# Kernel tuning notes

Measured on AMD Instinct MI355X. Metric: run time of the kernel, lower is better.

Reference implementation:

```python
import jax, jax.numpy as jnp
import numpy as np
from jax import lax

B, N, D = 16, 2048, 256
H = 64  # hidden_dim
EPS = 1e-5


def zero_softmax(x, eps=EPS):
    # zeros stay exactly zero: exp(0)-1 == 0
    e = jnp.exp(x) - 1.0
    return e / (jnp.sum(e, axis=-1, keepdims=True) + eps)


def setup_inputs() -> dict:
    key = jax.random.key(0)
    ks = jax.random.split(key, 9)
    s_in = 1.0 / np.sqrt(D)
    x = jax.random.normal(ks[0], (B, N, D), dtype=jnp.float32)
    Wq = jax.random.uniform(ks[1], (D, H), jnp.float32, -s_in, s_in)
    bq = jax.random.uniform(ks[2], (H,), jnp.float32, -s_in, s_in)
    Wk = jax.random.uniform(ks[3], (D, H), jnp.float32, -s_in, s_in)
    bk = jax.random.uniform(ks[4], (H,), jnp.float32, -s_in, s_in)
    Wv = jax.random.uniform(ks[5], (D, H), jnp.float32, -s_in, s_in)
    bv = jax.random.uniform(ks[6], (H,), jnp.float32, -s_in, s_in)
    s_c = 1.0 / 3.0  # conv fan_in = 1*3*3 = 9
    conv_w = jax.random.uniform(ks[7], (1, 1, 3, 3), jnp.float32, -s_c, s_c)
    conv_b = jax.random.uniform(ks[8], (1,), jnp.float32, -s_c, s_c)
    return {"x": x, "Wq": Wq, "bq": bq, "Wk": Wk, "bk": bk,
            "Wv": Wv, "bv": bv, "conv_w": conv_w, "conv_b": conv_b}


def reference(x, Wq, bq, Wk, bk, Wv, bv, conv_w, conv_b):
    scale = H ** (-0.5)
    q = jnp.einsum('bnd,dh->bnh', x, Wq) + bq
    k = jnp.einsum('bnd,dh->bnh', x, Wk) + bk
    v = jnp.einsum('bnd,dh->bnh', x, Wv) + bv
    A_dense = jnp.einsum('bnh,bmh->bnm', q, k) * scale  # [B, N, N]
    A_in = A_dense[:, None, :, :]  # [B, 1, N, N]
    A_conv = lax.conv_general_dilated(
        A_in, conv_w, window_strides=(1, 1), padding='SAME',
        dimension_numbers=('NCHW', 'OIHW', 'NCHW')) + conv_b[None, :, None, None]
    A_conv = jax.nn.sigmoid(A_conv)[:, 0, :, :]
    A_sparse = jax.nn.relu(A_dense - A_conv)
    A_norm = zero_softmax(A_sparse)
    return jnp.einsum('bnm,bmh->bnh', A_norm, v)
```

## Files before the change

kernel.cpp:

```cpp
#include <hip/hip_runtime.h>
#include <hip/hip_bf16.h>

typedef __bf16 bf16_t;
typedef __bf16 bf16x8 __attribute__((ext_vector_type(8)));
typedef float  floatx4 __attribute__((ext_vector_type(4)));

#define BQ 16
#define NTOK 2048
#define DIM 256
#define HD 64

__global__ __launch_bounds__(256) void k_prep(const float* __restrict__ Wq,
                                              const float* __restrict__ Wk,
                                              const float* __restrict__ Wv,
                                              bf16_t* __restrict__ wt) {
    int o = blockIdx.x * 256 + threadIdx.x;
    int w = o >> 14;
    int r = o & 16383;
    int h = r >> 8;
    int d = r & 255;
    const float* W = (w == 0) ? Wq : ((w == 1) ? Wk : Wv);
    wt[o] = (bf16_t)W[d * 64 + h];
}

#define XS 264
__global__ __launch_bounds__(256) void k_qkv(const float* __restrict__ x,
                                             const bf16_t* __restrict__ wt,
                                             const float* __restrict__ bq,
                                             const float* __restrict__ bk,
                                             const float* __restrict__ bv,
                                             bf16_t* __restrict__ qb,
                                             bf16_t* __restrict__ kb,
                                             bf16_t* __restrict__ vt) {
    __shared__ bf16_t x_ls[64 * XS];
    __shared__ bf16_t vt_ls[64 * 72];

    int b  = blockIdx.x >> 5;
    int t0 = (blockIdx.x & 31) << 6;
    int t  = threadIdx.x;
    int lane = t & 63;
    int w    = t >> 6;
    int m_   = lane & 15;
    int q4   = lane >> 4;

    for (int tau = t; tau < 4096; tau += 256) {
        int row = tau >> 6, ch = tau & 63;
        float4 v = ((const float4*)x)[(size_t)(b * NTOK + t0 + row) * 64 + ch];
        bf16_t tmp[4] = {(bf16_t)v.x, (bf16_t)v.y, (bf16_t)v.z, (bf16_t)v.w};
        *(uint2*)(&x_ls[row * XS + ch * 4]) = *(uint2*)tmp;
    }
    __syncthreads();

    for (int wi = 0; wi < 3; ++wi) {
        const bf16_t* wtw = wt + wi * 16384;
        floatx4 acc[4];
        #pragma unroll
        for (int mt = 0; mt < 4; ++mt) acc[mt] = floatx4{0.f, 0.f, 0.f, 0.f};

        #pragma unroll
        for (int ks = 0; ks < 8; ++ks) {
            bf16x8 bfrag = *(const bf16x8*)(wtw + (16 * w + m_) * 256 + ks * 32 + q4 * 8);
            #pragma unroll
            for (int mt = 0; mt < 4; ++mt) {
                bf16x8 afrag = *(const bf16x8*)(&x_ls[(16 * mt + m_) * XS + ks * 32 + q4 * 8]);
                acc[mt] = __builtin_amdgcn_mfma_f32_16x16x32_bf16(afrag, bfrag, acc[mt], 0, 0, 0);
            }
        }
        const float* bias_p = (wi == 0) ? bq : ((wi == 1) ? bk : bv);
        float bias = bias_p[16 * w + m_];
        float scale = (wi == 0) ? 0.125f : 1.0f;

        if (wi < 2) {
            bf16_t* dst = (wi == 0) ? qb : kb;
            #pragma unroll
            for (int mt = 0; mt < 4; ++mt)
                #pragma unroll
                for (int r = 0; r < 4; ++r) {
                    int tok = t0 + 16 * mt + 4 * q4 + r;
                    dst[(size_t)(b * NTOK + tok) * 64 + 16 * w + m_] = (bf16_t)((acc[mt][r] + bias) * scale);
                }
        } else {
            #pragma unroll
            for (int mt = 0; mt < 4; ++mt)
                #pragma unroll
                for (int r = 0; r < 4; ++r)
                    vt_ls[(16 * w + m_) * 72 + 16 * mt + 4 * q4 + r] = (bf16_t)(acc[mt][r] + bias);
            __syncthreads();
            for (int tau = t; tau < 512; tau += 256) {
                int h = tau >> 3, ch = tau & 7;
                uint4 val = *(const uint4*)(&vt_ls[h * 72 + ch * 8]);
                *(uint4*)(vt + (size_t)(b * 64 + h) * NTOK + t0 + ch * 8) = val;
            }
        }
    }
}

#define SA 52
#define SP 72
#define RINT 46
#define NITER 45
__global__ __launch_bounds__(256) void k_attn(const bf16_t* __restrict__ qb,
                                              const bf16_t* __restrict__ kb,
                                              const bf16_t* __restrict__ vt,
                                              const float* __restrict__ conv_w,
                                              const float* __restrict__ conv_b,
                                              float* __restrict__ out) {
    __shared__ bf16_t q_ls[48 * SP];
    __shared__ bf16_t k_ls[48 * SP];
    __shared__ bf16_t v_ls[64 * SP];
    __shared__ float  A_ls[48 * SA];
    __shared__ bf16_t p_ls[48 * SP];
    __shared__ float  rs_ls[48];

    int b  = blockIdx.y;
    int r0 = blockIdx.x * RINT;
    int t = threadIdx.x, lane = t & 63, w = t >> 6;
    int m_ = lane & 15, q4 = lane >> 4;

    const uint* vt32 = (const uint*)vt + (size_t)b * 64 * 1024;

    int vh[6], vc[6];
    #pragma unroll
    for (int j = 0; j < 6; ++j) { int tau = t + 256 * j; vh[j] = tau / 23; vc[j] = tau % 23; }

    float cw[9];
    #pragma unroll
    for (int i = 0; i < 9; ++i) cw[i] = conv_w[i];
    float cb = conv_b[0];

    uint4 kreg[2];
    uint  vreg[6];
    auto prefetch = [&](int c0) {
        {
            int row = t >> 3, ch = t & 7;
            int g = c0 - 1 + row;
            uint4 val = make_uint4(0u, 0u, 0u, 0u);
            if (g >= 0 && g < NTOK)
                val = *(const uint4*)(kb + (size_t)(b * NTOK + g) * 64 + ch * 8);
            kreg[0] = val;
        }
        if (t < 128) {
            int row = (t + 256) >> 3, ch = t & 7;
            int g = c0 - 1 + row;
            uint4 val = make_uint4(0u, 0u, 0u, 0u);
            if (g >= 0 && g < NTOK)
                val = *(const uint4*)(kb + (size_t)(b * NTOK + g) * 64 + ch * 8);
            kreg[1] = val;
        }
        #pragma unroll
        for (int j = 0; j < 6; ++j) {
            if (t + 256 * j < 1472) {
                int n = c0 + 2 * vc[j];
                uint val = 0u;
                if (n < NTOK) val = vt32[vh[j] * 1024 + (n >> 1)];
                vreg[j] = val;
            }
        }
    };

    prefetch(0);

    for (int u = t; u < 1728; u += 256) ((uint*)p_ls)[u] = 0u;
    for (int u = t; u < 1152; u += 256) {
        int h = u / 18, c = 46 + u % 18;
        v_ls[h * SP + c] = (bf16_t)0.f;
    }
    if (t < 192) A_ls[(t >> 2) * SA + 48 + (t & 3)] = 0.f;
    for (int tau = t; tau < 384; tau += 256) {
        int row = tau >> 3, ch = tau & 7;
        int g = r0 - 1 + row;
        uint4 val = make_uint4(0u, 0u, 0u, 0u);
        if (g >= 0 && g < NTOK)
            val = *(const uint4*)(qb + (size_t)(b * NTOK + g) * 64 + ch * 8);
        *(uint4*)(&q_ls[row * SP + ch * 8]) = val;
    }

    floatx4 accO[3];
    #pragma unroll
    for (int ti = 0; ti < 3; ++ti) accO[ti] = floatx4{0.f, 0.f, 0.f, 0.f};
    float rs[3] = {0.f, 0.f, 0.f};

    for (int it = 0; it < NITER; ++it) {
        {
            int row = t >> 3, ch = t & 7;
            *(uint4*)(&k_ls[row * SP + ch * 8]) = kreg[0];
            if (t < 128) {
                int row1 = (t + 256) >> 3;
                *(uint4*)(&k_ls[row1 * SP + ch * 8]) = kreg[1];
            }
            #pragma unroll
            for (int j = 0; j < 6; ++j)
                if (t + 256 * j < 1472)
                    *(uint*)(&v_ls[vh[j] * SP + 2 * vc[j]]) = vreg[j];
        }
        __syncthreads();

        for (int T = w; T < 9; T += 4) {
            int ti = T / 3, tj = T % 3;
            floatx4 a = floatx4{0.f, 0.f, 0.f, 0.f};
            #pragma unroll
            for (int ks = 0; ks < 2; ++ks) {
                bf16x8 af = *(const bf16x8*)(&q_ls[(16 * ti + m_) * SP + ks * 32 + q4 * 8]);
                bf16x8 bf = *(const bf16x8*)(&k_ls[(16 * tj + m_) * SP + ks * 32 + q4 * 8]);
                a = __builtin_amdgcn_mfma_f32_16x16x32_bf16(af, bf, a, 0, 0, 0);
            }
            #pragma unroll
            for (int r = 0; r < 4; ++r)
                A_ls[(16 * ti + 4 * q4 + r) * SA + 16 * tj + m_] = a[r];
        }
        __syncthreads();

        if (it + 1 < NITER) prefetch((it + 1) * RINT);

        #pragma unroll
        for (int round = 0; round < 3; ++round) {
            int idx = t + (round << 8);
            if (idx < 552) {
                int i = idx / 12 + 1;
                int g = idx - (i - 1) * 12;
                const float* base = &A_ls[(i - 1) * SA + 4 * g];
                float a0[6], a1[6], a2[6];
                *(float4*)(a0) = *(const float4*)(base);
                *(float2*)(a0 + 4) = *(const float2*)(base + 4);
                *(float4*)(a1) = *(const float4*)(base + SA);
                *(float2*)(a1 + 4) = *(const float2*)(base + SA + 4);
                *(float4*)(a2) = *(const float4*)(base + 2 * SA);
                *(float2*)(a2 + 4) = *(const float2*)(base + 2 * SA + 4);
                float esum = 0.f;
                bf16_t quad[4];
                #pragma unroll
                for (int x = 0; x < 4; ++x) {
                    float conv = cb
                        + cw[0] * a0[x] + cw[1] * a0[x + 1] + cw[2] * a0[x + 2]
                        + cw[3] * a1[x] + cw[4] * a1[x + 1] + cw[5] * a1[x + 2]
                        + cw[6] * a2[x] + cw[7] * a2[x + 1] + cw[8] * a2[x + 2];
                    float sig = __builtin_amdgcn_rcpf(1.f + __expf(-conv));
                    float s = fmaxf(a1[x + 1] - sig, 0.f);
                    float ev = __expf(s) - 1.f;
                    if (4 * g + x > 45) ev = 0.f;
                    quad[x] = (bf16_t)ev;
                    esum += ev;
                }
                rs[round] += esum;
                *(uint2*)(&p_ls[i * SP + 4 * g]) = *(uint2*)quad;
            }
        }
        __syncthreads();

        #pragma unroll
        for (int ks = 0; ks < 2; ++ks) {
            bf16x8 bf = *(const bf16x8*)(&v_ls[(16 * w + m_) * SP + ks * 32 + q4 * 8]);
            #pragma unroll
            for (int ti = 0; ti < 3; ++ti) {
                bf16x8 af = *(const bf16x8*)(&p_ls[(16 * ti + m_) * SP + ks * 32 + q4 * 8]);
                accO[ti] = __builtin_amdgcn_mfma_f32_16x16x32_bf16(af, bf, accO[ti], 0, 0, 0);
            }
        }
        __syncthreads();
    }

    float* sc = A_ls;
    sc[t * 3 + 0] = rs[0];
    sc[t * 3 + 1] = rs[1];
    sc[t * 3 + 2] = rs[2];
    __syncthreads();
    if (t < 46) {
        float s = 0.f;
        #pragma unroll
        for (int j = 0; j < 12; ++j) {
            int idx = 12 * t + j;
            s += sc[(idx & 255) * 3 + (idx >> 8)];
        }
        rs_ls[t + 1] = s + 1e-5f;
    }
    __syncthreads();

    #pragma unroll
    for (int ti = 0; ti < 3; ++ti) {
        #pragma unroll
        for (int r = 0; r < 4; ++r) {
            int i = 16 * ti + 4 * q4 + r;
            int grow = r0 + i - 1;
            if (i >= 1 && i < 47 && grow < NTOK)
                out[(size_t)(b * NTOK + grow) * 64 + 16 * w + m_] = accO[ti][r] / rs_ls[i];
        }
    }
}

extern "C" void kernel_launch(void* const* d_in, const int* in_sizes, int n_in,
                              void* d_out, int out_size, void* d_ws, size_t ws_size,
                              hipStream_t stream) {
    const float* x  = (const float*)d_in[0];
    const float* Wq = (const float*)d_in[1];
    const float* bq = (const float*)d_in[2];
    const float* Wk = (const float*)d_in[3];
    const float* bk = (const float*)d_in[4];
    const float* Wv = (const float*)d_in[5];
    const float* bv = (const float*)d_in[6];
    const float* cw = (const float*)d_in[7];
    const float* cb = (const float*)d_in[8];
    float* out = (float*)d_out;

    char* ws = (char*)d_ws;
    bf16_t* wt = (bf16_t*)ws;
    bf16_t* qb = (bf16_t*)(ws + 98304);
    bf16_t* kb = (bf16_t*)(ws + 98304 + 4194304);
    bf16_t* vt = (bf16_t*)(ws + 98304 + 8388608);

    k_prep<<<dim3(192), dim3(256), 0, stream>>>(Wq, Wk, Wv, wt);
    k_qkv<<<dim3(512), dim3(256), 0, stream>>>(x, wt, bq, bk, bv, qb, kb, vt);
    k_attn<<<dim3(NITER, BQ), dim3(256), 0, stream>>>(qb, kb, vt, cw, cb, out);
}
```

Measured before the change: 231.9 us.

## Split attention key dimension across three blocks with atomic accumulation and normalization pass

The attention kernel's loop over key chunks is split three ways into separate blocks (grid 45x3x16), raising the block count from 720 to 2160 so more CUs are occupied. Partial outputs and row sums are combined with float atomicAdd into a zeroed output and row-sum buffer. Zeroing is folded into the prep kernel, and a new kernel divides by the row sum afterwards. This costs extra atomic traffic, an extra pass over the output, and a nondeterministic summation order.

Measured after the change: 226.8 us. 2.2% less time.

```diff
diff --git a/kernel.cpp b/kernel.cpp
--- a/kernel.cpp
+++ b/kernel.cpp
@@ -13,14 +13,23 @@
 __global__ __launch_bounds__(256) void k_prep(const float* __restrict__ Wq,
                                               const float* __restrict__ Wk,
                                               const float* __restrict__ Wv,
-                                              bf16_t* __restrict__ wt) {
+                                              bf16_t* __restrict__ wt,
+                                              float* __restrict__ outz,
+                                              float* __restrict__ rsz) {
     int o = blockIdx.x * 256 + threadIdx.x;
-    int w = o >> 14;
-    int r = o & 16383;
-    int h = r >> 8;
-    int d = r & 255;
-    const float* W = (w == 0) ? Wq : ((w == 1) ? Wk : Wv);
-    wt[o] = (bf16_t)W[d * 64 + h];
+    if (o < 49152) {
+        int w = o >> 14;
+        int r = o & 16383;
+        int h = r >> 8;
+        int d = r & 255;
+        const float* W = (w == 0) ? Wq : ((w == 1) ? Wk : Wv);
+        wt[o] = (bf16_t)W[d * 64 + h];
+    }
+    float4 z = make_float4(0.f, 0.f, 0.f, 0.f);
+    for (int u = o; u < 532480; u += 262144) {
+        if (u < 524288) ((float4*)outz)[u] = z;
+        else            ((float4*)rsz)[u - 524288] = z;
+    }
 }
 
 #define XS 264
@@ -98,22 +107,23 @@
 #define SA 52
 #define SP 72
 #define RINT 46
-#define NITER 45
+#define NIT_C 15
 __global__ __launch_bounds__(256) void k_attn(const bf16_t* __restrict__ qb,
                                               const bf16_t* __restrict__ kb,
                                               const bf16_t* __restrict__ vt,
                                               const float* __restrict__ conv_w,
                                               const float* __restrict__ conv_b,
-                                              float* __restrict__ out) {
+                                              float* __restrict__ outp,
+                                              float* __restrict__ rsg) {
     __shared__ bf16_t q_ls[48 * SP];
     __shared__ bf16_t k_ls[48 * SP];
     __shared__ bf16_t v_ls[64 * SP];
     __shared__ float  A_ls[48 * SA];
     __shared__ bf16_t p_ls[48 * SP];
-    __shared__ float  rs_ls[48];
-
-    int b  = blockIdx.y;
-    int r0 = blockIdx.x * RINT;
+
+    int b    = blockIdx.z;
+    int r0   = blockIdx.x * RINT;
+    int ch0  = blockIdx.y * NIT_C;
     int t = threadIdx.x, lane = t & 63, w = t >> 6;
     int m_ = lane & 15, q4 = lane >> 4;
 
@@ -158,7 +168,7 @@
         }
     };
 
-    prefetch(0);
+    prefetch(ch0 * RINT);
 
     for (int u = t; u < 1728; u += 256) ((uint*)p_ls)[u] = 0u;
     for (int u = t; u < 1152; u += 256) {
@@ -180,7 +190,7 @@
     for (int ti = 0; ti < 3; ++ti) accO[ti] = floatx4{0.f, 0.f, 0.f, 0.f};
     float rs[3] = {0.f, 0.f, 0.f};
 
-    for (int it = 0; it < NITER; ++it) {
+    for (int it = 0; it < NIT_C; ++it) {
         {
             int row = t >> 3, ch = t & 7;
             *(uint4*)(&k_ls[row * SP + ch * 8]) = kreg[0];
@@ -210,7 +220,7 @@
         }
         __syncthreads();
 
-        if (it + 1 < NITER) prefetch((it + 1) * RINT);
+        if (it + 1 < NIT_C) prefetch((ch0 + it + 1) * RINT);
 
         #pragma unroll
         for (int round = 0; round < 3; ++round) {
@@ -264,16 +274,16 @@
     sc[t * 3 + 1] = rs[1];
     sc[t * 3 + 2] = rs[2];
     __syncthreads();
-    if (t < 46) {
+    if (t < RINT) {
         float s = 0.f;
         #pragma unroll
         for (int j = 0; j < 12; ++j) {
             int idx = 12 * t + j;
             s += sc[(idx & 255) * 3 + (idx >> 8)];
         }
-        rs_ls[t + 1] = s + 1e-5f;
-    }
-    __syncthreads();
+        int grow = r0 + t;
+        if (grow < NTOK) atomicAdd(&rsg[b * NTOK + grow], s);
+    }
 
     #pragma unroll
     for (int ti = 0; ti < 3; ++ti) {
@@ -282,9 +292,19 @@
             int i = 16 * ti + 4 * q4 + r;
             int grow = r0 + i - 1;
             if (i >= 1 && i < 47 && grow < NTOK)
-                out[(size_t)(b * NTOK + grow) * 64 + 16 * w + m_] = accO[ti][r] / rs_ls[i];
-        }
-    }
+                atomicAdd(&outp[((size_t)(b * NTOK + grow) << 6) + 16 * w + m_], accO[ti][r]);
+        }
+    }
+}
+
+__global__ __launch_bounds__(256) void k_norm(float* __restrict__ out,
+                                              const float* __restrict__ rsg) {
+    int gid = blockIdx.x * 256 + threadIdx.x;
+    float4 o = ((float4*)out)[gid];
+    float d = rsg[gid >> 4] + 1e-5f;
+    float inv = 1.f / d;
+    o.x *= inv; o.y *= inv; o.z *= inv; o.w *= inv;
+    ((float4*)out)[gid] = o;
 }
 
 extern "C" void kernel_launch(void* const* d_in, const int* in_sizes, int n_in,
@@ -306,8 +326,10 @@
     bf16_t* qb = (bf16_t*)(ws + 98304);
     bf16_t* kb = (bf16_t*)(ws + 98304 + 4194304);
     bf16_t* vt = (bf16_t*)(ws + 98304 + 8388608);
-
-    k_prep<<<dim3(192), dim3(256), 0, stream>>>(Wq, Wk, Wv, wt);
+    float*  rsg = (float*)(ws + 98304 + 12582912);
+
+    k_prep<<<dim3(1024), dim3(256), 0, stream>>>(Wq, Wk, Wv, wt, out, rsg);
     k_qkv<<<dim3(512), dim3(256), 0, stream>>>(x, wt, bq, bk, bv, qb, kb, vt);
-    k_attn<<<dim3(NITER, BQ), dim3(256), 0, stream>>>(qb, kb, vt, cw, cb, out);
-}
+    k_attn<<<dim3(45, 3, BQ), dim3(256), 0, stream>>>(qb, kb, vt, cw, cb, out, rsg);
+    k_norm<<<dim3(2048), dim3(256), 0, stream>>>(out, rsg);
+}
```
